# Kernel optimization log

Hardware: AMD Instinct MI355X
Metric: run time of the kernel (lower is better)

Reference implementation:

```python
import jax, jax.numpy as jnp
import numpy as np

HID = 4096
N_HEADS = 32
N_KV_HEADS = 8
HEAD_DIM = HID // N_HEADS  # 128
Q_SIZE = N_HEADS * HEAD_DIM
KV_SIZE = N_KV_HEADS * HEAD_DIM
ROPE_THETA = 10000.0
SCALE = HEAD_DIM ** -0.5


def setup_inputs() -> dict:
    key = jax.random.key(0)
    k1, k2, k3 = jax.random.split(key, 3)
    B, S = 1, 2048
    hidden_states = jax.random.normal(k1, (B, S, HID), dtype=jnp.float32)
    positions = jnp.broadcast_to(jnp.arange(S, dtype=jnp.int32)[None, :], (B, S))
    w_qkv = jax.random.normal(k2, (HID, Q_SIZE + 2 * KV_SIZE), dtype=jnp.float32) * 0.02
    w_o = jax.random.normal(k3, (Q_SIZE, HID), dtype=jnp.float32) * 0.02
    return {"positions": positions, "hidden_states": hidden_states,
            "w_qkv": w_qkv, "w_o": w_o}


def _rotate_half(x):
    x1, x2 = jnp.split(x, 2, axis=-1)
    return jnp.concatenate([-x2, x1], axis=-1)


def _apply_rope(x, cos, sin):
    # x: [B,S,H,D], cos/sin: [B,S,D]
    return x * cos[:, :, None, :] + _rotate_half(x) * sin[:, :, None, :]


def reference(positions, hidden_states, w_qkv, w_o):
    B, S, _ = hidden_states.shape
    # fused QKV projection
    qkv = hidden_states @ w_qkv  # [B,S,6144]
    q = qkv[..., :Q_SIZE].reshape(B, S, N_HEADS, HEAD_DIM)
    k = qkv[..., Q_SIZE:Q_SIZE + KV_SIZE].reshape(B, S, N_KV_HEADS, HEAD_DIM)
    v = qkv[..., Q_SIZE + KV_SIZE:].reshape(B, S, N_KV_HEADS, HEAD_DIM)

    # NeoX-style rotary embedding over full head_dim
    inv_freq = 1.0 / (ROPE_THETA ** (jnp.arange(0, HEAD_DIM, 2, dtype=jnp.float32) / HEAD_DIM))
    angles = positions.astype(jnp.float32)[..., None] * inv_freq  # [B,S,D/2]
    emb = jnp.concatenate([angles, angles], axis=-1)  # [B,S,D]
    cos, sin = jnp.cos(emb), jnp.sin(emb)
    q = _apply_rope(q, cos, sin)
    k = _apply_rope(k, cos, sin)

    # GQA: expand kv heads to match query heads
    rep = N_HEADS // N_KV_HEADS
    k = jnp.repeat(k, rep, axis=2)  # [B,S,H,D]
    v = jnp.repeat(v, rep, axis=2)

    # causal attention
    scores = jnp.einsum('bqhd,bkhd->bhqk', q, k) * SCALE  # [B,H,S,S]
    causal = jnp.tril(jnp.ones((S, S), dtype=bool))
    scores = jnp.where(causal[None, None], scores, jnp.finfo(scores.dtype).min)
    probs = jax.nn.softmax(scores, axis=-1)
    attn = jnp.einsum('bhqk,bkhd->bqhd', probs, v).reshape(B, S, Q_SIZE)

    return attn @ w_o  # [B,S,HID]
```

## Files before the change

### kernel.cpp

```cpp
#include <hip/hip_runtime.h>
#include <cmath>

typedef __bf16 bf16_t;
typedef __bf16 bf16x8 __attribute__((ext_vector_type(8)));
typedef float  f32x4  __attribute__((ext_vector_type(4)));

#define SEQ    2048
#define HID    4096
#define QKV_N  6144
#define NH     32
#define NKV    8
#define HD     128
#define ATT_SCALE 0.08838834764831845f

__device__ __forceinline__ f32x4 mfma16(bf16x8 a, bf16x8 b, f32x4 c) {
  return __builtin_amdgcn_mfma_f32_16x16x32_bf16(a, b, c, 0, 0, 0);
}

__device__ __forceinline__ void gload_lds16(const void* g, void* l) {
  __builtin_amdgcn_global_load_lds(
      (const __attribute__((address_space(1))) void*)g,
      (__attribute__((address_space(3))) void*)l, 16, 0, 0);
}

__global__ __launch_bounds__(256) void cast_f32_bf16(
    const float* __restrict__ in, bf16_t* __restrict__ out, int n) {
  int i = (blockIdx.x * 256 + threadIdx.x) * 8;
  if (i >= n) return;
  float4 v0 = *(const float4*)(in + i);
  float4 v1 = *(const float4*)(in + i + 4);
  bf16x8 o;
  o[0] = (bf16_t)v0.x; o[1] = (bf16_t)v0.y; o[2] = (bf16_t)v0.z; o[3] = (bf16_t)v0.w;
  o[4] = (bf16_t)v1.x; o[5] = (bf16_t)v1.y; o[6] = (bf16_t)v1.z; o[7] = (bf16_t)v1.w;
  *(bf16x8*)(out + i) = o;
}

__global__ __launch_bounds__(256) void transpose_cast(
    const float* __restrict__ in, bf16_t* __restrict__ out, int R, int C) {
  __shared__ float tile[32][33];
  int c0 = blockIdx.x * 32, r0 = blockIdx.y * 32;
  int x = threadIdx.x, y = threadIdx.y;
  for (int j = 0; j < 32; j += 8)
    tile[y + j][x] = in[(size_t)(r0 + y + j) * C + c0 + x];
  __syncthreads();
  for (int j = 0; j < 32; j += 8)
    out[(size_t)(c0 + y + j) * R + r0 + x] = (bf16_t)tile[x][y + j];
}

__global__ __launch_bounds__(256) void transpose_v(
    const bf16_t* __restrict__ qkv, bf16_t* __restrict__ vt) {
  __shared__ bf16_t tile[32][33];
  int c0 = blockIdx.x * 32, r0 = blockIdx.y * 32;
  int x = threadIdx.x, y = threadIdx.y;
  for (int j = 0; j < 32; j += 8)
    tile[y + j][x] = qkv[(size_t)(r0 + y + j) * QKV_N + 5120 + c0 + x];
  __syncthreads();
  for (int j = 0; j < 32; j += 8)
    vt[(size_t)(c0 + y + j) * SEQ + r0 + x] = tile[x][y + j];
}

__global__ __launch_bounds__(256) void rope_tables(
    const int* __restrict__ pos, float* __restrict__ ct, float* __restrict__ st) {
  int idx = blockIdx.x * 256 + threadIdx.x;
  if (idx >= SEQ * 64) return;
  int s = idx >> 6, j = idx & 63;
  double inv = exp(-((double)(2 * j) / 128.0) * log(10000.0));
  double a = (double)pos[s] * inv;
  ct[idx] = (float)cos(a);
  st[idx] = (float)sin(a);
}

__global__ __launch_bounds__(256) void rope_apply(
    bf16_t* __restrict__ qkv, const float* __restrict__ ct, const float* __restrict__ st) {
  int idx = blockIdx.x * 256 + threadIdx.x;
  int s = idx / 2560, p = idx % 2560;
  int head = p >> 6, j = p & 63;
  int base = (head < NH) ? head * HD : HID + (head - NH) * HD;
  size_t o1 = (size_t)s * QKV_N + base + j;
  float x1 = (float)qkv[o1], x2 = (float)qkv[o1 + 64];
  float c = ct[s * 64 + j], sn = st[s * 64 + j];
  qkv[o1]      = (bf16_t)(x1 * c - x2 * sn);
  qkv[o1 + 64] = (bf16_t)(x2 * c + x1 * sn);
}

template <typename OutT>
__global__ __launch_bounds__(256, 2) void gemm_bt(
    const bf16_t* __restrict__ A, const bf16_t* __restrict__ Bt,
    OutT* __restrict__ C, int M, int N, int K) {
  __shared__ bf16_t As[128 * 32];
  __shared__ bf16_t Bs[128 * 32];
  const int tid = threadIdx.x;
  const int wid = tid >> 6, lane = tid & 63;
  const int m0 = blockIdx.y * 128, n0 = blockIdx.x * 128;
  const int wr = (wid >> 1) * 64, wc = (wid & 1) * 64;
  const int lrow = lane & 15, lk = lane >> 4;
  f32x4 acc[4][4];
  for (int m = 0; m < 4; ++m)
    for (int n = 0; n < 4; ++n) acc[m][n] = f32x4{0.f, 0.f, 0.f, 0.f};

  for (int k0 = 0; k0 < K; k0 += 32) {
    for (int i = 0; i < 2; ++i) {
      int off = wid * 2048 + i * 1024 + lane * 16;
      int row = off >> 6;
      int kk = (off & 63) >> 1;
      gload_lds16(A + (size_t)(m0 + row) * K + k0 + kk,
                  (char*)As + wid * 2048 + i * 1024);
      gload_lds16(Bt + (size_t)(n0 + row) * K + k0 + kk,
                  (char*)Bs + wid * 2048 + i * 1024);
    }
    __syncthreads();
    bf16x8 a[4], b[4];
    for (int m = 0; m < 4; ++m)
      a[m] = *(const bf16x8*)(As + (wr + m * 16 + lrow) * 32 + lk * 8);
    for (int n = 0; n < 4; ++n)
      b[n] = *(const bf16x8*)(Bs + (wc + n * 16 + lrow) * 32 + lk * 8);
    for (int m = 0; m < 4; ++m)
      for (int n = 0; n < 4; ++n)
        acc[m][n] = mfma16(a[m], b[n], acc[m][n]);
    __syncthreads();
  }
  for (int m = 0; m < 4; ++m)
    for (int n = 0; n < 4; ++n)
      for (int r = 0; r < 4; ++r) {
        int row = m0 + wr + m * 16 + lk * 4 + r;
        int col = n0 + wc + n * 16 + lrow;
        C[(size_t)row * N + col] = (OutT)acc[m][n][r];
      }
}

__global__ __launch_bounds__(256) void flash_attn(
    const bf16_t* __restrict__ qkv, const bf16_t* __restrict__ vt,
    bf16_t* __restrict__ attn_out) {
  __shared__ bf16_t Ks[64 * 128];
  __shared__ bf16_t Vs[128 * 64];
  __shared__ bf16_t Ps[4][32 * 64];
  const int h = blockIdx.x, qb = blockIdx.y;
  const int q0 = qb * 128, kvh = h >> 2;
  const int tid = threadIdx.x, wid = tid >> 6, lane = tid & 63;
  const int lrow = lane & 15, lk = lane >> 4;

  bf16x8 qreg[2][4];
  for (int m = 0; m < 2; ++m) {
    int qr = q0 + wid * 32 + m * 16 + lrow;
    for (int kd = 0; kd < 4; ++kd)
      qreg[m][kd] =
          *(const bf16x8*)(qkv + (size_t)qr * QKV_N + h * HD + kd * 32 + lk * 8);
  }

  f32x4 acc[2][8];
  float mst[2][4], lst[2][4];
  for (int m = 0; m < 2; ++m) {
    for (int df = 0; df < 8; ++df) acc[m][df] = f32x4{0.f, 0.f, 0.f, 0.f};
    for (int r = 0; r < 4; ++r) { mst[m][r] = -1e30f; lst[m][r] = 0.f; }
  }

  const int ntiles = (q0 + 128) / 64;
  for (int t = 0; t < ntiles; ++t) {
    const int kv0 = t * 64;
    __syncthreads();
    for (int rnd = 0; rnd < 4; ++rnd) {
      int ch = rnd * 256 + tid, r = ch >> 4, c = ch & 15;
      bf16x8 v = *(const bf16x8*)(qkv + (size_t)(kv0 + r) * QKV_N + HID +
                                  kvh * HD + c * 8);
      *(bf16x8*)((char*)Ks + ((r * 256 + c * 16) ^ ((r & 7) << 4))) = v;
    }
    for (int rnd = 0; rnd < 4; ++rnd) {
      int ch = rnd * 256 + tid, d = ch >> 3, c = ch & 7;
      bf16x8 v =
          *(const bf16x8*)(vt + (size_t)(kvh * HD + d) * SEQ + kv0 + c * 8);
      *(bf16x8*)((char*)Vs + ((d * 128 + c * 16) ^ ((d & 7) << 4))) = v;
    }
    __syncthreads();

    f32x4 s[2][4];
    for (int m = 0; m < 2; ++m)
      for (int n = 0; n < 4; ++n) s[m][n] = f32x4{0.f, 0.f, 0.f, 0.f};
    for (int kd = 0; kd < 4; ++kd) {
      bf16x8 kf[4];
      for (int n = 0; n < 4; ++n) {
        int kr = n * 16 + lrow;
        kf[n] = *(const bf16x8*)((char*)Ks +
                                 ((kr * 256 + kd * 64 + lk * 16) ^ ((kr & 7) << 4)));
      }
      for (int m = 0; m < 2; ++m)
        for (int n = 0; n < 4; ++n)
          s[m][n] = mfma16(qreg[m][kd], kf[n], s[m][n]);
    }

    for (int m = 0; m < 2; ++m) {
      int qrow = q0 + wid * 32 + m * 16 + lk * 4;
      for (int r = 0; r < 4; ++r) {
        int qg = qrow + r;
        float mx = -1e30f;
        for (int n = 0; n < 4; ++n) {
          float val = s[m][n][r] * ATT_SCALE;
          if (kv0 + n * 16 + lrow > qg) val = -1e30f;
          s[m][n][r] = val;
          mx = fmaxf(mx, val);
        }
        for (int off = 1; off < 16; off <<= 1) mx = fmaxf(mx, __shfl_xor(mx, off));
        float mnew = fmaxf(mst[m][r], mx);
        float alpha = __expf(mst[m][r] - mnew);
        float rs = 0.f;
        for (int n = 0; n < 4; ++n) {
          float p = __expf(s[m][n][r] - mnew);
          s[m][n][r] = p;
          rs += p;
        }
        for (int off = 1; off < 16; off <<= 1) rs += __shfl_xor(rs, off);
        lst[m][r] = lst[m][r] * alpha + rs;
        mst[m][r] = mnew;
        for (int df = 0; df < 8; ++df) acc[m][df][r] *= alpha;
      }
    }

    bf16_t* ps = &Ps[wid][0];
    for (int m = 0; m < 2; ++m)
      for (int n = 0; n < 4; ++n)
        for (int r = 0; r < 4; ++r) {
          int row = m * 16 + lk * 4 + r, col = n * 16 + lrow;
          *(bf16_t*)((char*)ps + ((row * 128 + col * 2) ^ ((row & 7) << 4))) =
              (bf16_t)s[m][n][r];
        }

    for (int kc = 0; kc < 2; ++kc) {
      bf16x8 pa[2];
      for (int m = 0; m < 2; ++m) {
        int row = m * 16 + lrow;
        pa[m] = *(const bf16x8*)((char*)ps +
                                 ((row * 128 + kc * 64 + lk * 16) ^ ((row & 7) << 4)));
      }
      for (int df = 0; df < 8; ++df) {
        int d = df * 16 + lrow;
        bf16x8 vb = *(const bf16x8*)((char*)Vs +
                                     ((d * 128 + kc * 64 + lk * 16) ^ ((d & 7) << 4)));
        for (int m = 0; m < 2; ++m) acc[m][df] = mfma16(pa[m], vb, acc[m][df]);
      }
    }
  }

  for (int m = 0; m < 2; ++m)
    for (int r = 0; r < 4; ++r) {
      float inv = 1.f / lst[m][r];
      int row = q0 + wid * 32 + m * 16 + lk * 4 + r;
      for (int df = 0; df < 8; ++df) {
        int col = h * HD + df * 16 + lrow;
        attn_out[(size_t)row * HID + col] = (bf16_t)(acc[m][df][r] * inv);
      }
    }
}

extern "C" void kernel_launch(void* const* d_in, const int* in_sizes, int n_in,
                              void* d_out, int out_size, void* d_ws, size_t ws_size,
                              hipStream_t stream) {
  const int*   positions = (const int*)d_in[0];
  const float* hs        = (const float*)d_in[1];
  const float* wqkv      = (const float*)d_in[2];
  const float* wo        = (const float*)d_in[3];
  float*       out       = (float*)d_out;
  char* ws = (char*)d_ws;

  bf16_t* hsb   = (bf16_t*)(ws + 0);
  bf16_t* wqkvt = (bf16_t*)(ws + 16777216);
  bf16_t* wot   = (bf16_t*)(ws + 67108864);
  bf16_t* qkv   = (bf16_t*)(ws + 100663296);
  float*  ct    = (float*)(ws + 125829120);
  float*  st    = (float*)(ws + 126353408);
  bf16_t* vtb   = (bf16_t*)(ws + 126877696);
  bf16_t* attn  = (bf16_t*)(ws + 131072000);

  cast_f32_bf16<<<4096, 256, 0, stream>>>(hs, hsb, SEQ * HID);
  transpose_cast<<<dim3(192, 128), dim3(32, 8), 0, stream>>>(wqkv, wqkvt, HID, QKV_N);
  transpose_cast<<<dim3(128, 128), dim3(32, 8), 0, stream>>>(wo, wot, HID, HID);
  rope_tables<<<512, 256, 0, stream>>>(positions, ct, st);

  gemm_bt<bf16_t><<<dim3(48, 16), 256, 0, stream>>>(hsb, wqkvt, qkv, SEQ, QKV_N, HID);

  rope_apply<<<20480, 256, 0, stream>>>(qkv, ct, st);
  transpose_v<<<dim3(32, 64), dim3(32, 8), 0, stream>>>(qkv, vtb);

  flash_attn<<<dim3(NH, SEQ / 128), 256, 0, stream>>>(qkv, vtb, attn);

  gemm_bt<float><<<dim3(32, 16), 256, 0, stream>>>(attn, wot, out, SEQ, HID, HID);
}
```

Before: 606.8 us.

## Restructure flash attention into single-wave blocks reading K/V directly from global

Flash attention now runs one 64-thread wave per 32-row query block, launched heaviest-first, so causal work is split into finer units. K and V fragments are loaded straight from global memory instead of being staged in shared memory, which removes block-wide barriers but relies on cache hits. Masking is applied only on diagonal tiles, and the running max is rescaled only when it grows by more than a threshold (lazy rescaling), cutting exp and multiply work per tile. Finer blocks and direct global loads may raise memory traffic and lower reuse across query rows.

```diff
diff --git a/kernel.cpp b/kernel.cpp
--- a/kernel.cpp
+++ b/kernel.cpp
@@ -128,20 +128,20 @@
       }
 }
 
-__global__ __launch_bounds__(256) void flash_attn(
+__global__ __launch_bounds__(64, 3) void flash_attn(
     const bf16_t* __restrict__ qkv, const bf16_t* __restrict__ vt,
     bf16_t* __restrict__ attn_out) {
-  __shared__ bf16_t Ks[64 * 128];
-  __shared__ bf16_t Vs[128 * 64];
-  __shared__ bf16_t Ps[4][32 * 64];
-  const int h = blockIdx.x, qb = blockIdx.y;
-  const int q0 = qb * 128, kvh = h >> 2;
-  const int tid = threadIdx.x, wid = tid >> 6, lane = tid & 63;
+  __shared__ bf16_t Ps[32 * 64];
+  const int h = blockIdx.x;
+  const int j = 63 - (int)blockIdx.y;
+  const int q0 = j * 32;
+  const int kvh = h >> 2;
+  const int lane = threadIdx.x;
   const int lrow = lane & 15, lk = lane >> 4;
 
   bf16x8 qreg[2][4];
   for (int m = 0; m < 2; ++m) {
-    int qr = q0 + wid * 32 + m * 16 + lrow;
+    int qr = q0 + m * 16 + lrow;
     for (int kd = 0; kd < 4; ++kd)
       qreg[m][kd] =
           *(const bf16x8*)(qkv + (size_t)qr * QKV_N + h * HD + kd * 32 + lk * 8);
@@ -154,72 +154,58 @@
     for (int r = 0; r < 4; ++r) { mst[m][r] = -1e30f; lst[m][r] = 0.f; }
   }
 
-  const int ntiles = (q0 + 128) / 64;
+  const int ntiles = (q0 + 95) >> 6;
   for (int t = 0; t < ntiles; ++t) {
     const int kv0 = t * 64;
-    __syncthreads();
-    for (int rnd = 0; rnd < 4; ++rnd) {
-      int ch = rnd * 256 + tid, r = ch >> 4, c = ch & 15;
-      bf16x8 v = *(const bf16x8*)(qkv + (size_t)(kv0 + r) * QKV_N + HID +
-                                  kvh * HD + c * 8);
-      *(bf16x8*)((char*)Ks + ((r * 256 + c * 16) ^ ((r & 7) << 4))) = v;
-    }
-    for (int rnd = 0; rnd < 4; ++rnd) {
-      int ch = rnd * 256 + tid, d = ch >> 3, c = ch & 7;
-      bf16x8 v =
-          *(const bf16x8*)(vt + (size_t)(kvh * HD + d) * SEQ + kv0 + c * 8);
-      *(bf16x8*)((char*)Vs + ((d * 128 + c * 16) ^ ((d & 7) << 4))) = v;
-    }
-    __syncthreads();
 
     f32x4 s[2][4];
     for (int m = 0; m < 2; ++m)
       for (int n = 0; n < 4; ++n) s[m][n] = f32x4{0.f, 0.f, 0.f, 0.f};
     for (int kd = 0; kd < 4; ++kd) {
       bf16x8 kf[4];
-      for (int n = 0; n < 4; ++n) {
-        int kr = n * 16 + lrow;
-        kf[n] = *(const bf16x8*)((char*)Ks +
-                                 ((kr * 256 + kd * 64 + lk * 16) ^ ((kr & 7) << 4)));
-      }
+      for (int n = 0; n < 4; ++n)
+        kf[n] = *(const bf16x8*)(qkv + (size_t)(kv0 + n * 16 + lrow) * QKV_N +
+                                 HID + kvh * HD + kd * 32 + lk * 8);
       for (int m = 0; m < 2; ++m)
         for (int n = 0; n < 4; ++n)
           s[m][n] = mfma16(qreg[m][kd], kf[n], s[m][n]);
     }
 
+    const bool needMask = (kv0 + 63 > q0);
+
     for (int m = 0; m < 2; ++m) {
-      int qrow = q0 + wid * 32 + m * 16 + lk * 4;
       for (int r = 0; r < 4; ++r) {
-        int qg = qrow + r;
-        float mx = -1e30f;
+        const int qg = q0 + m * 16 + lk * 4 + r;
+        float v[4];
         for (int n = 0; n < 4; ++n) {
           float val = s[m][n][r] * ATT_SCALE;
-          if (kv0 + n * 16 + lrow > qg) val = -1e30f;
-          s[m][n][r] = val;
-          mx = fmaxf(mx, val);
-        }
+          if (needMask && (kv0 + n * 16 + lrow > qg)) val = -1e30f;
+          v[n] = val;
+        }
+        float mx = fmaxf(fmaxf(v[0], v[1]), fmaxf(v[2], v[3]));
         for (int off = 1; off < 16; off <<= 1) mx = fmaxf(mx, __shfl_xor(mx, off));
-        float mnew = fmaxf(mst[m][r], mx);
-        float alpha = __expf(mst[m][r] - mnew);
+        if (mx > mst[m][r] + 8.f) {
+          float alpha = __expf(mst[m][r] - mx);
+          mst[m][r] = mx;
+          lst[m][r] *= alpha;
+          for (int df = 0; df < 8; ++df) acc[m][df][r] *= alpha;
+        }
         float rs = 0.f;
         for (int n = 0; n < 4; ++n) {
-          float p = __expf(s[m][n][r] - mnew);
+          float p = __expf(v[n] - mst[m][r]);
           s[m][n][r] = p;
           rs += p;
         }
         for (int off = 1; off < 16; off <<= 1) rs += __shfl_xor(rs, off);
-        lst[m][r] = lst[m][r] * alpha + rs;
-        mst[m][r] = mnew;
-        for (int df = 0; df < 8; ++df) acc[m][df][r] *= alpha;
-      }
-    }
-
-    bf16_t* ps = &Ps[wid][0];
+        lst[m][r] += rs;
+      }
+    }
+
     for (int m = 0; m < 2; ++m)
       for (int n = 0; n < 4; ++n)
         for (int r = 0; r < 4; ++r) {
           int row = m * 16 + lk * 4 + r, col = n * 16 + lrow;
-          *(bf16_t*)((char*)ps + ((row * 128 + col * 2) ^ ((row & 7) << 4))) =
+          *(bf16_t*)((char*)Ps + ((row * 128 + col * 2) ^ ((row & 7) << 4))) =
               (bf16_t)s[m][n][r];
         }
 
@@ -227,13 +213,13 @@
       bf16x8 pa[2];
       for (int m = 0; m < 2; ++m) {
         int row = m * 16 + lrow;
-        pa[m] = *(const bf16x8*)((char*)ps +
+        pa[m] = *(const bf16x8*)((char*)Ps +
                                  ((row * 128 + kc * 64 + lk * 16) ^ ((row & 7) << 4)));
       }
       for (int df = 0; df < 8; ++df) {
-        int d = df * 16 + lrow;
-        bf16x8 vb = *(const bf16x8*)((char*)Vs +
-                                     ((d * 128 + kc * 64 + lk * 16) ^ ((d & 7) << 4)));
+        int d = kvh * HD + df * 16 + lrow;
+        bf16x8 vb =
+            *(const bf16x8*)(vt + (size_t)d * SEQ + kv0 + kc * 32 + lk * 8);
         for (int m = 0; m < 2; ++m) acc[m][df] = mfma16(pa[m], vb, acc[m][df]);
       }
     }
@@ -242,7 +228,7 @@
   for (int m = 0; m < 2; ++m)
     for (int r = 0; r < 4; ++r) {
       float inv = 1.f / lst[m][r];
-      int row = q0 + wid * 32 + m * 16 + lk * 4 + r;
+      int row = q0 + m * 16 + lk * 4 + r;
       for (int df = 0; df < 8; ++df) {
         int col = h * HD + df * 16 + lrow;
         attn_out[(size_t)row * HID + col] = (bf16_t)(acc[m][df][r] * inv);
@@ -279,7 +265,7 @@
   rope_apply<<<20480, 256, 0, stream>>>(qkv, ct, st);
   transpose_v<<<dim3(32, 64), dim3(32, 8), 0, stream>>>(qkv, vtb);
 
-  flash_attn<<<dim3(NH, SEQ / 128), 256, 0, stream>>>(qkv, vtb, attn);
+  flash_attn<<<dim3(NH, 64), 64, 0, stream>>>(qkv, vtb, attn);
 
   gemm_bt<float><<<dim3(32, 16), 256, 0, stream>>>(attn, wot, out, SEQ, HID, HID);
 }
```

Result: slower. 939.1 us (+54.8%).
